# Optimization experiments

Hardware: AMD Instinct MI355X
Metric: run time of the kernel (lower is better)

## Reference

```python
import jax, jax.numpy as jnp
import numpy as np

B, N, K, H = 8, 1024, 16, 4
EMB = 1024

def lrelu(x):
    return jnp.where(x >= 0, x, 0.2 * x)

def bn(x, g, b):
    # eval-mode BatchNorm with running_mean=0, running_var=1
    inv = 1.0 / np.sqrt(1.0 + 1e-5)
    shape = (1, -1) + (1,) * (x.ndim - 2)
    return x * (g * inv).reshape(shape) + b.reshape(shape)

def conv1x1(x, w):
    # 1x1 conv == channel matmul; x: (B,C,...), w: (O,C)
    return jnp.einsum('bc...,oc->bo...', x, w)

def knn_idx(x, k):
    # x: (B,C,N); negative squared pairwise distance, top-k largest = nearest
    inner = -2.0 * jnp.einsum('bcn,bcm->bnm', x, x)
    xx = jnp.sum(x * x, axis=1)                      # (B,N)
    pd = -xx[:, :, None] - inner - xx[:, None, :]
    return jax.lax.top_k(pd, k)[1]                   # (B,N,k)

def graph_feature(x, idx):
    b = x.shape[0]
    xt = jnp.transpose(x, (0, 2, 1))                 # (B,N,C)
    nbr = xt[jnp.arange(b)[:, None, None], idx]      # (B,N,K,C) gather
    ctr = jnp.broadcast_to(xt[:, :, None, :], nbr.shape)
    f = jnp.concatenate([nbr - ctr, ctr], axis=-1)   # (B,N,K,2C)
    return jnp.transpose(f, (0, 3, 1, 2))            # (B,2C,N,K)

def mak(x, y, w0, g0, b0, wm, gm, bm, w1, go, bo, ws, gs, bs, out_ch, in_ch):
    # Multi-head adaptive kernel: generate per-point (out,in,H) weights from y, apply to x
    Bc, _, Nc, Kc = x.shape
    y = lrelu(bn(conv1x1(y, w0), g0, b0))
    y = lrelu(bn(conv1x1(y, wm), gm, bm))
    y = conv1x1(y, w1)                               # (B, out*in*H, N, K)
    w = jnp.transpose(y, (0, 2, 3, 1)).reshape(Bc, Nc, Kc, out_ch, in_ch, H)
    xt = jnp.transpose(x, (0, 2, 3, 1))              # (B,N,K,in)
    # per-head matmul then sum over heads == single einsum over i and h
    out = jnp.einsum('bnkoih,bnki->bonk', w, xt)
    out = bn(out, go, bo)
    idt = bn(conv1x1(x, ws), gs, bs)                 # shortcut (in != out)
    return lrelu(out + idt)


def setup_inputs() -> dict:
    ks = jax.random.split(jax.random.key(0), 48)
    it = iter(range(48))
    def nrm(shape, fan):
        return jax.random.normal(ks[next(it)], shape, jnp.float32) / np.sqrt(fan)
    def gam(c):
        return jax.random.uniform(ks[next(it)], (c,), jnp.float32, 0.5, 1.5)
    def bet(c):
        return 0.1 * jax.random.normal(ks[next(it)], (c,), jnp.float32)
    d = {}
    d['x'] = jax.random.normal(ks[next(it)], (B, 3, N), jnp.float32)
    def mak_params(p, feat_c):
        d[p + '_w0'] = nrm((64, feat_c), feat_c); d[p + '_g0'] = gam(64); d[p + '_b0'] = bet(64)
        d[p + '_wm'] = nrm((64, 64), 64); d[p + '_gm'] = gam(64); d[p + '_bm'] = bet(64)
        d[p + '_w1'] = nrm((64 * 6 * H, 64), 64)
        d[p + '_go'] = gam(64); d[p + '_bo'] = bet(64)
        d[p + '_ws'] = nrm((64, 6), 6); d[p + '_gs'] = gam(64); d[p + '_bs'] = bet(64)
    mak_params('m1', 6)
    mak_params('m2', 128)
    d['w3'] = nrm((128, 128), 128); d['g3'] = gam(128); d['b3'] = bet(128)
    d['w4'] = nrm((256, 256), 256); d['g4'] = gam(256); d['b4'] = bet(256)
    d['w5'] = nrm((EMB, 512), 512); d['g5'] = gam(EMB); d['b5'] = bet(EMB)
    d['wl1'] = nrm((512, 2 * EMB), 2 * EMB); d['bn4_g'] = gam(512); d['bn4_b'] = bet(512)
    d['wl2'] = nrm((256, 512), 512); d['bl2'] = bet(256); d['bn5_g'] = gam(256); d['bn5_b'] = bet(256)
    d['wl3'] = nrm((49, 256), 256); d['bl3'] = bet(49)
    return d


def reference(x, m1_w0, m1_g0, m1_b0, m1_wm, m1_gm, m1_bm, m1_w1, m1_go, m1_bo, m1_ws, m1_gs, m1_bs, m2_w0, m2_g0, m2_b0, m2_wm, m2_gm, m2_bm, m2_w1, m2_go, m2_bo, m2_ws, m2_gs, m2_bs, w3, g3, b3, w4, g4, b4, w5, g5, b5, wl1, bn4_g, bn4_b, wl2, bl2, bn5_g, bn5_b, wl3, bl3):
    idx = knn_idx(x, K)                              # common_idx from points
    geo = graph_feature(x, idx)                      # (B,6,N,K); feat_x == geo_x at stage 1
    h = mak(geo, geo, m1_w0, m1_g0, m1_b0, m1_wm, m1_gm, m1_bm, m1_w1, m1_go, m1_bo, m1_ws, m1_gs, m1_bs, 64, 6)
    x1 = h.max(axis=-1)                              # (B,64,N)
    feat2 = graph_feature(x1, idx)                   # (B,128,N,K)
    h = mak(geo, feat2, m2_w0, m2_g0, m2_b0, m2_wm, m2_gm, m2_bm, m2_w1, m2_go, m2_bo, m2_ws, m2_gs, m2_bs, 64, 6)
    x2 = h.max(axis=-1)                              # (B,64,N)
    x3 = lrelu(bn(conv1x1(graph_feature(x2, idx), w3), g3, b3)).max(axis=-1)   # (B,128,N)
    x4 = lrelu(bn(conv1x1(graph_feature(x3, idx), w4), g4, b4)).max(axis=-1)   # (B,256,N)
    xc = jnp.concatenate([x1, x2, x3, x4], axis=1)   # (B,512,N)
    x5 = lrelu(bn(conv1x1(xc, w5), g5, b5))          # (B,EMB,N)
    xp = jnp.concatenate([x5.max(axis=-1), x5.mean(axis=-1)], axis=1)  # (B,2*EMB)
    xf = lrelu(bn(xp @ wl1.T, bn4_g, bn4_b))
    xf = lrelu(bn(xf @ wl2.T + bl2, bn5_g, bn5_b))
    return xf @ wl3.T + bl3                           # (B,49)
```

## Files before the change

### kernel.cpp

```cpp
#include <hip/hip_runtime.h>
#include <math.h>

#define BB 8
#define NN 1024
#define KK 16
#define NKP (NN*KK)
#define BN_INV 0.99999500003749981f

typedef unsigned short u16;
typedef __attribute__((ext_vector_type(8))) short short8;
typedef __attribute__((ext_vector_type(4))) float f32x4;

#define MFMA16(a,b,c) __builtin_amdgcn_mfma_f32_16x16x32_bf16(a,b,c,0,0,0)

__device__ __forceinline__ float lrelu(float v) { return v >= 0.f ? v : 0.2f * v; }

__device__ __forceinline__ u16 f2bf(float f) {
  union { float f; unsigned u; } v; v.f = f;
  unsigned r = v.u + 0x7fff + ((v.u >> 16) & 1);
  return (u16)(r >> 16);
}
__device__ __forceinline__ float bf2f(u16 s) {
  union { unsigned u; float f; } v; v.u = ((unsigned)s) << 16;
  return v.f;
}

constexpr size_t OFF_IDX   = 0;
constexpr size_t OFF_X1P   = 524288;
constexpr size_t OFF_X2P   = 1572864;
constexpr size_t OFF_X3P   = 2621440;
constexpr size_t OFF_MUV   = 2621440;
constexpr size_t OFF_X4P   = 4718592;
constexpr size_t OFF_GEO   = 4718592;
constexpr size_t OFF_PMAX  = 8912896;
constexpr size_t OFF_PSUM  = 9437184;
constexpr size_t OFF_XP    = 9961472;
constexpr size_t OFF_XF1   = 10027008;
constexpr size_t OFF_XF2   = 10043392;
constexpr size_t OFF_M1WM  = 10055680;
constexpr size_t OFF_M1W1S = 10063872;
constexpr size_t OFF_M2W0S = 10117120;
constexpr size_t OFF_M2WM  = 10133504;
constexpr size_t OFF_M2W1S = 10141696;
constexpr size_t OFF_W3S   = 10194944;
constexpr size_t OFF_W4S   = 10227712;
constexpr size_t OFF_W5    = 10358784;
constexpr size_t OFF_WL1T  = 11407360;
constexpr size_t OFF_WL2T  = 15601664;
constexpr size_t OFF_WL3T  = 16125952;
constexpr size_t OFF_UV3   = 16177152;
constexpr size_t OFF_EY0   = 16177152;
constexpr size_t OFF_UV4   = 20371456;

struct SSeg { const float* w; const float* g; u16* dst; int O; int C; int cpl2; int ch; int stk; int start; };
struct SArgs { SSeg seg[6]; int total; };

__global__ __launch_bounds__(256) void prep_scale_bf16(SArgs a) {
  const int tid = blockIdx.x * 256 + threadIdx.x;
  if (tid >= a.total) return;
  int s = 0;
  #pragma unroll
  for (int i = 1; i < 6; ++i) if (tid >= a.seg[i].start) s = i;
  const SSeg sg = a.seg[s];
  const int e = tid - sg.start;
  const int o2 = e >> sg.cpl2;
  const int c = e & ((1 << sg.cpl2) - 1);
  float v = 0.f;
  if (sg.stk) {
    const int half = sg.O >> 1;
    const int o = o2 & (half - 1);
    const int CIN = 2 * sg.C;
    const float wd = sg.w[o * CIN + c];
    v = (o2 < half) ? wd : (sg.w[o * CIN + sg.C + c] - wd);
    v *= sg.g[o] * BN_INV;
  } else if (c < sg.C) {
    v = sg.w[o2 * sg.C + c];
    if (sg.ch && c >= sg.ch) v -= sg.w[o2 * sg.C + c - sg.ch];
    v *= sg.g[o2] * BN_INV;
  }
  sg.dst[(size_t)(c >> 5) * (sg.O * 32) + o2 * 32 + (c & 31)] = f2bf(v);
}

__global__ __launch_bounds__(256) void prep_w1s_bf16(
    const float* __restrict__ w1a, const float* __restrict__ wsa,
    const float* __restrict__ goa, const float* __restrict__ gsa,
    const float* __restrict__ w1b, const float* __restrict__ wsb,
    const float* __restrict__ gob, const float* __restrict__ gsb,
    u16* __restrict__ dsta, u16* __restrict__ dstb) {
  const int tid = blockIdx.x * 256 + threadIdx.x;
  if (tid >= 64 * 416) return;
  const float* w1 = blockIdx.y ? w1b : w1a;
  const float* wsm = blockIdx.y ? wsb : wsa;
  const float* go = blockIdx.y ? gob : goa;
  const float* gs = blockIdx.y ? gsb : gsa;
  u16* dst = blockIdx.y ? dstb : dsta;
  const int o = tid / 416, ci = tid - o * 416;
  float v = 0.f;
  if (ci < 384) {
    const int ii = ci >> 6, ch = ci & 63;
    const int base = (o * 24 + ii * 4) * 64 + ch;
    v = go[o] * BN_INV * (w1[base] + w1[base + 64] + w1[base + 128] + w1[base + 192]);
  } else if (ci < 390) {
    v = gs[o] * BN_INV * wsm[o * 6 + (ci - 384)];
  }
  dst[(size_t)(ci >> 5) * 2048 + o * 32 + (ci & 31)] = f2bf(v);
}

struct TSeg { const float* w; const float* g; float* dst; int O; int C; int start; };
struct TArgs3 { TSeg seg[3]; int total; };

__global__ __launch_bounds__(256) void prep_transpose_f32(TArgs3 a) {
  const int tid = blockIdx.x * 256 + threadIdx.x;
  if (tid >= a.total) return;
  int s = 0;
  #pragma unroll
  for (int i = 1; i < 3; ++i) if (tid >= a.seg[i].start) s = i;
  const TSeg sg = a.seg[s];
  const int e = tid - sg.start;
  const int c = e / sg.O;
  const int o = e - c * sg.O;
  float v = sg.w[o * sg.C + c];
  if (sg.g) v *= sg.g[o] * BN_INV;
  sg.dst[e] = v;
}

__global__ __launch_bounds__(256) void knn_kernel(const float* __restrict__ x, int* __restrict__ idxout) {
  const int wid  = (blockIdx.x * blockDim.x + threadIdx.x) >> 6;
  const int lane = threadIdx.x & 63;
  const int b = wid >> 10;
  const int n = wid & (NN - 1);
  const float* xb = x + b * 3 * NN;
  const float x0n = xb[n], x1n = xb[NN + n], x2n = xb[2 * NN + n];
  const float xxn = x0n * x0n + x1n * x1n + x2n * x2n;
  float pd[16];
  #pragma unroll
  for (int j = 0; j < 16; ++j) {
    const int m = j * 64 + lane;
    const float x0 = xb[m], x1 = xb[NN + m], x2 = xb[2 * NN + m];
    const float dot = x0n * x0 + x1n * x1 + x2n * x2;
    const float xxm = x0 * x0 + x1 * x1 + x2 * x2;
    pd[j] = 2.f * dot - xxn - xxm;
  }
  for (int r = 0; r < 16; ++r) {
    float bv = pd[0]; int bj = 0;
    #pragma unroll
    for (int j = 1; j < 16; ++j) if (pd[j] > bv) { bv = pd[j]; bj = j; }
    int bm = bj * 64 + lane;
    #pragma unroll
    for (int off = 32; off > 0; off >>= 1) {
      const float ov = __shfl_down(bv, off);
      const int   om = __shfl_down(bm, off);
      if (ov > bv || (ov == bv && om < bm)) { bv = ov; bm = om; }
    }
    bm = __shfl(bm, 0);
    if (lane == 0) idxout[wid * KK + r] = bm;
    const int  cj   = bm >> 6;
    const bool mine = (bm & 63) == lane;
    #pragma unroll
    for (int j = 0; j < 16; ++j) if (mine && j == cj) pd[j] = -INFINITY;
  }
}

__device__ __forceinline__ short8 bfrag64(const u16* T, int pl, int quad, int c0) {
  const int pos = ((c0 >> 3) + quad) ^ (pl & 7);
  return *(const short8*)(T + pl * 64 + pos * 8);
}
__device__ __forceinline__ void writeD64(u16* T, int pl, int quad, const f32x4 a,
                                         const float* __restrict__ bias, int obase) {
  union { ushort4 v; u16 s[4]; } pk;
  #pragma unroll
  for (int r = 0; r < 4; ++r) pk.s[r] = f2bf(lrelu(a[r] + bias[obase + quad * 4 + r]));
  const int g = (obase + quad * 4) >> 3;
  const int pos = g ^ (pl & 7);
  *(ushort4*)(T + pl * 64 + pos * 8 + (quad & 1) * 4) = pk.v;
}

__global__ __launch_bounds__(256) void mak1_uv(
    const float* __restrict__ x, const float* __restrict__ w0,
    const float* __restrict__ g0, const float* __restrict__ b0,
    u16* __restrict__ MUV) {
  const int tid = blockIdx.x * 256 + threadIdx.x;
  if (tid >= BB * NN * 64) return;
  const int o = tid & 63;
  const int p = tid >> 6;
  const int b = p >> 10, n = p & (NN - 1);
  const float* xb = x + b * 3 * NN;
  const float gg = g0[o] * BN_INV;
  float u = 0.f, v = 0.f;
  #pragma unroll
  for (int i = 0; i < 3; ++i) {
    const float wd = w0[o * 6 + i];
    const float wc = w0[o * 6 + 3 + i];
    const float c = xb[i * NN + n];
    u += wd * c;
    v += (wc - wd) * c;
  }
  MUV[(size_t)p * 128 + o]      = f2bf(gg * u);
  MUV[(size_t)p * 128 + 64 + o] = f2bf(gg * v + b0[o]);
}

__global__ __launch_bounds__(256) void mak_edge_build(
    const float* __restrict__ x, const int* __restrict__ idxb,
    const u16* __restrict__ MUV, u16* __restrict__ EY0,
    u16* __restrict__ GEO, int writeGeo) {
  const int tid = blockIdx.x * 256 + threadIdx.x;
  const int cg = tid & 7;
  const int e = tid >> 3;
  const int b = e >> 14;
  const int nk = e & 16383;
  const int n = nk >> 4;
  const int nbr = idxb[e] & (NN - 1);
  union { uint4 q; u16 s[8]; } uu, vv, rr;
  uu.q = *(const uint4*)(MUV + (size_t)(b * NN + nbr) * 128 + cg * 8);
  vv.q = *(const uint4*)(MUV + (size_t)(b * NN + n) * 128 + 64 + cg * 8);
  #pragma unroll
  for (int j = 0; j < 8; ++j) rr.s[j] = f2bf(lrelu(bf2f(uu.s[j]) + bf2f(vv.s[j])));
  *(uint4*)(EY0 + (size_t)e * 64 + cg * 8) = rr.q;
  if (writeGeo && cg == 0) {
    const float* xb = x + b * 3 * NN;
    union { uint4 q; u16 s[8]; } g;
    #pragma unroll
    for (int i = 0; i < 3; ++i) {
      const float fc = xb[i * NN + n];
      g.s[i]     = f2bf(xb[i * NN + nbr] - fc);
      g.s[3 + i] = f2bf(fc);
    }
    g.s[6] = 0; g.s[7] = 0;
    *(uint4*)(GEO + (size_t)e * 8) = g.q;
  }
}

__global__ __launch_bounds__(256, 2) void mak23_mfma(
    const u16* __restrict__ EY0, const u16* __restrict__ GEO,
    const u16* __restrict__ wmb, const float* __restrict__ bmv,
    const u16* __restrict__ w1s, const float* __restrict__ bov, const float* __restrict__ bsv,
    u16* __restrict__ Xoutp) {
  __shared__ __align__(16) u16 YMs[4][64 * 64];

  const int t = threadIdx.x;
  const int b = blockIdx.z;
  const int w = t >> 6, l = t & 63;
  const int quad = l >> 4, l15 = l & 15;
  const int cq8 = quad * 8;
  const int p0 = blockIdx.x * 16 + w * 4;
  u16* myYM = YMs[w];

  float ge[4][6];
  short8 bgv[4];
  size_t eL[4];
  #pragma unroll
  for (int pg = 0; pg < 4; ++pg) {
    eL[pg] = ((size_t)(b * NN + p0 + pg)) * 16 + l15;
    union { short8 v; u16 s[8]; } gq;
    gq.v = *(const short8*)(GEO + eL[pg] * 8);
    #pragma unroll
    for (int ii = 0; ii < 6; ++ii) ge[pg][ii] = bf2f(gq.s[ii]);
    bgv[pg] = (quad == 0) ? gq.v : (short8)(short)0;
  }

  #pragma unroll
  for (int pg = 0; pg < 4; ++pg) {
    f32x4 a2[4];
    #pragma unroll
    for (int i = 0; i < 4; ++i) a2[i] = (f32x4)0.f;
    #pragma unroll
    for (int kc = 0; kc < 2; ++kc) {
      const short8 bf = *(const short8*)(EY0 + eL[pg] * 64 + kc * 32 + cq8);
      #pragma unroll
      for (int at = 0; at < 4; ++at) {
        const short8 af = *(const short8*)(wmb + (size_t)(kc * 64 + at * 16 + l15) * 32 + cq8);
        a2[at] = MFMA16(af, bf, a2[at]);
      }
    }
    #pragma unroll
    for (int at = 0; at < 4; ++at) writeD64(myYM, pg * 16 + l15, quad, a2[at], bmv, at * 16);
  }

  short8 bf3[4][2];
  #pragma unroll
  for (int pg = 0; pg < 4; ++pg)
    #pragma unroll
    for (int kc = 0; kc < 2; ++kc)
      bf3[pg][kc] = bfrag64(myYM, pg * 16 + l15, quad, kc * 32);

  f32x4 acc[4][4];
  #pragma unroll
  for (int pg = 0; pg < 4; ++pg)
    #pragma unroll
    for (int at = 0; at < 4; ++at) acc[pg][at] = (f32x4)0.f;

  #pragma unroll
  for (int ii = 0; ii < 6; ++ii) {
    f32x4 tac[4][4];
    #pragma unroll
    for (int pg = 0; pg < 4; ++pg)
      #pragma unroll
      for (int at = 0; at < 4; ++at) tac[pg][at] = (f32x4)0.f;
    #pragma unroll
    for (int kc = 0; kc < 2; ++kc) {
      #pragma unroll
      for (int at = 0; at < 4; ++at) {
        const short8 af = *(const short8*)(w1s + (size_t)((ii * 2 + kc) * 64 + at * 16 + l15) * 32 + cq8);
        #pragma unroll
        for (int pg = 0; pg < 4; ++pg) tac[pg][at] = MFMA16(af, bf3[pg][kc], tac[pg][at]);
      }
    }
    #pragma unroll
    for (int pg = 0; pg < 4; ++pg) {
      const float g = ge[pg][ii];
      #pragma unroll
      for (int at = 0; at < 4; ++at) acc[pg][at] += g * tac[pg][at];
    }
  }
  #pragma unroll
  for (int at = 0; at < 4; ++at) {
    const short8 af = *(const short8*)(w1s + (size_t)(12 * 64 + at * 16 + l15) * 32 + cq8);
    #pragma unroll
    for (int pg = 0; pg < 4; ++pg) acc[pg][at] = MFMA16(af, bgv[pg], acc[pg][at]);
  }

  #pragma unroll
  for (int pg = 0; pg < 4; ++pg) {
    u16* orow = Xoutp + (size_t)(b * NN + p0 + pg) * 64;
    #pragma unroll
    for (int at = 0; at < 4; ++at) {
      union { ushort4 v; u16 s[4]; } pk;
      #pragma unroll
      for (int r = 0; r < 4; ++r) {
        const int o = at * 16 + quad * 4 + r;
        float v = lrelu(acc[pg][at][r] + bov[o] + bsv[o]);
        v = fmaxf(v, __shfl_xor(v, 1));
        v = fmaxf(v, __shfl_xor(v, 2));
        v = fmaxf(v, __shfl_xor(v, 4));
        v = fmaxf(v, __shfl_xor(v, 8));
        pk.s[r] = f2bf(v);
      }
      if (l15 == 0) *(ushort4*)(orow + at * 16 + quad * 4) = pk.v;
    }
  }
}

template<int CH, int COUT2>
__global__ __launch_bounds__(256) void dense_uv(
    const u16* __restrict__ srcp, const u16* __restrict__ w2,
    const float* __restrict__ bias, u16* __restrict__ UV) {
  constexpr int COUT = COUT2 / 2;
  constexpr int NCH = CH / 32;
  const int t = threadIdx.x;
  const int b = blockIdx.z;
  const int w = t >> 6, l = t & 63;
  const int quad = l >> 4, l15 = l & 15;
  const int cq8 = quad * 8;
  int n0, ow0;
  if constexpr (COUT2 >= 256) { n0 = blockIdx.x * 64; ow0 = blockIdx.y * 256 + w * 64; }
  else { n0 = blockIdx.x * 128 + (w >> 1) * 64; ow0 = (w & 1) * 64; }

  f32x4 acc[4][4];
  #pragma unroll
  for (int i = 0; i < 4; ++i)
    #pragma unroll
    for (int j = 0; j < 4; ++j) acc[i][j] = (f32x4)0.f;

  #pragma unroll
  for (int k = 0; k < NCH; ++k) {
    short8 bfr[4];
    #pragma unroll
    for (int pg = 0; pg < 4; ++pg) {
      const int n = n0 + pg * 16 + l15;
      bfr[pg] = *(const short8*)(srcp + (size_t)(b * NN + n) * CH + k * 32 + cq8);
    }
    #pragma unroll
    for (int at = 0; at < 4; ++at) {
      const short8 af = *(const short8*)(w2 + ((size_t)(k * COUT2 + ow0 + at * 16 + l15)) * 32 + cq8);
      #pragma unroll
      for (int pg = 0; pg < 4; ++pg) acc[at][pg] = MFMA16(af, bfr[pg], acc[at][pg]);
    }
  }

  #pragma unroll
  for (int at = 0; at < 4; ++at) {
    const int o0 = ow0 + at * 16 + quad * 4;
    const bool isv = (o0 >= COUT);
    float bb[4];
    #pragma unroll
    for (int r = 0; r < 4; ++r) bb[r] = isv ? bias[o0 + r - COUT] : 0.f;
    #pragma unroll
    for (int pg = 0; pg < 4; ++pg) {
      const int n = n0 + pg * 16 + l15;
      union { ushort4 v; u16 s[4]; } pk;
      #pragma unroll
      for (int r = 0; r < 4; ++r) pk.s[r] = f2bf(acc[at][pg][r] + bb[r]);
      *(ushort4*)(UV + (size_t)(b * NN + n) * COUT2 + o0) = pk.v;
    }
  }
}

__device__ __forceinline__ float4 ubf4(ushort4 q) {
  float4 f;
  f.x = bf2f(q.x); f.y = bf2f(q.y); f.z = bf2f(q.z); f.w = bf2f(q.w);
  return f;
}

template<int COUT>
__global__ __launch_bounds__(256) void gather_max(
    const u16* __restrict__ UV, const int* __restrict__ idxb,
    u16* __restrict__ Xoutp) {
  constexpr int CG = COUT / 4;
  const int tid = blockIdx.x * 256 + threadIdx.x;
  const int cg = tid & (CG - 1);
  const int P = tid / CG;
  const int b = P >> 10;
  const int n = P & (NN - 1);

  const float4 vv = ubf4(*(const ushort4*)(UV + (size_t)P * (2 * COUT) + COUT + 4 * cg));
  const int4* ip = (const int4*)(idxb + (size_t)b * NKP + n * 16);
  float4 m = {-INFINITY, -INFINITY, -INFINITY, -INFINITY};
  #pragma unroll
  for (int kq = 0; kq < 4; ++kq) {
    const int4 iv = ip[kq];
    const int mr[4] = { iv.x & (NN - 1), iv.y & (NN - 1), iv.z & (NN - 1), iv.w & (NN - 1) };
    ushort4 uq[4];
    #pragma unroll
    for (int j = 0; j < 4; ++j)
      uq[j] = *(const ushort4*)(UV + (size_t)(b * NN + mr[j]) * (2 * COUT) + 4 * cg);
    #pragma unroll
    for (int j = 0; j < 4; ++j) {
      const float4 uu = ubf4(uq[j]);
      float4 s;
      s.x = uu.x + vv.x; s.y = uu.y + vv.y; s.z = uu.z + vv.z; s.w = uu.w + vv.w;
      m.x = fmaxf(m.x, fmaxf(s.x, 0.2f * s.x));
      m.y = fmaxf(m.y, fmaxf(s.y, 0.2f * s.y));
      m.z = fmaxf(m.z, fmaxf(s.z, 0.2f * s.z));
      m.w = fmaxf(m.w, fmaxf(s.w, 0.2f * s.w));
    }
  }
  union { ushort4 v; u16 s[4]; } pk;
  pk.s[0] = f2bf(m.x); pk.s[1] = f2bf(m.y); pk.s[2] = f2bf(m.z); pk.s[3] = f2bf(m.w);
  *(ushort4*)(Xoutp + (size_t)P * COUT + 4 * cg) = pk.v;
}

__global__ __launch_bounds__(256) void conv5_mfma(
    const u16* __restrict__ X1P, const u16* __restrict__ X2P,
    const u16* __restrict__ X3P, const u16* __restrict__ X4P,
    const u16* __restrict__ w5b, const float* __restrict__ b5,
    float* __restrict__ PMAX, float* __restrict__ PSUM) {
  const int t = threadIdx.x;
  const int b = blockIdx.z;
  const int n0 = blockIdx.x * 64;
  const int w = t >> 6, l = t & 63;
  const int quad = l >> 4, l15 = l & 15;
  const int cq8 = quad * 8;
  const int ow0 = blockIdx.y * 256 + w * 64;

  f32x4 acc[4][4];
  #pragma unroll
  for (int i = 0; i < 4; ++i)
    #pragma unroll
    for (int j = 0; j < 4; ++j) acc[i][j] = (f32x4)0.f;

  #pragma unroll 4
  for (int k = 0; k < 16; ++k) {
    const int c = k * 32 + cq8;
    short8 bfr[4];
    #pragma unroll
    for (int pg = 0; pg < 4; ++pg) {
      const int n = n0 + pg * 16 + l15;
      const u16* src; int cc;
      if (c < 64)       { src = X1P + (size_t)(b * NN + n) * 64;  cc = c; }
      else if (c < 128) { src = X2P + (size_t)(b * NN + n) * 64;  cc = c - 64; }
      else if (c < 256) { src = X3P + (size_t)(b * NN + n) * 128; cc = c - 128; }
      else              { src = X4P + (size_t)(b * NN + n) * 256; cc = c - 256; }
      bfr[pg] = *(const short8*)(src + cc);
    }
    #pragma unroll
    for (int at = 0; at < 4; ++at) {
      const short8 af = *(const short8*)(w5b + ((size_t)(k * 1024 + ow0 + at * 16 + l15)) * 32 + cq8);
      #pragma unroll
      for (int pg = 0; pg < 4; ++pg) acc[at][pg] = MFMA16(af, bfr[pg], acc[at][pg]);
    }
  }

  #pragma unroll
  for (int at = 0; at < 4; ++at) {
    f32x4 pmx, psm;
    #pragma unroll
    for (int r = 0; r < 4; ++r) {
      const float bb = b5[ow0 + at * 16 + quad * 4 + r];
      float m = -INFINITY, s = 0.f;
      #pragma unroll
      for (int pg = 0; pg < 4; ++pg) {
        const float v = lrelu(acc[at][pg][r] + bb);
        m = fmaxf(m, v); s += v;
      }
      #pragma unroll
      for (int msk = 1; msk < 16; msk <<= 1) {
        m = fmaxf(m, __shfl_xor(m, msk));
        s += __shfl_xor(s, msk);
      }
      pmx[r] = m; psm[r] = s;
    }
    if (l15 == 0) {
      float* dm = PMAX + (size_t)(b * 16 + blockIdx.x) * 1024 + ow0 + at * 16 + quad * 4;
      float* ds = PSUM + (size_t)(b * 16 + blockIdx.x) * 1024 + ow0 + at * 16 + quad * 4;
      *(f32x4*)dm = pmx;
      *(f32x4*)ds = psm;
    }
  }
}

__global__ __launch_bounds__(256) void reduce5(const float* __restrict__ PMAX, const float* __restrict__ PSUM,
                                               float* __restrict__ XPg) {
  const int tid = blockIdx.x * 256 + threadIdx.x;
  const int b = tid >> 10, o = tid & 1023;
  float m = -INFINITY, s = 0.f;
  for (int pt = 0; pt < 16; ++pt) {
    m = fmaxf(m, PMAX[(size_t)(b * 16 + pt) * 1024 + o]);
    s += PSUM[(size_t)(b * 16 + pt) * 1024 + o];
  }
  XPg[b * 2048 + o] = m;
  XPg[b * 2048 + 1024 + o] = s * (1.f / 1024.f);
}

__global__ __launch_bounds__(256) void fc1_kernel(const float* __restrict__ XPg, const float* __restrict__ wl1t,
                                                  const float* __restrict__ bn4_b, float* __restrict__ XF1) {
  __shared__ float red[64 * 5];
  const int t = threadIdx.x;
  const int b = blockIdx.y;
  const int o = blockIdx.x * 64 + (t & 63);
  const int cq = t >> 6;
  const float* xp = XPg + b * 2048;
  float acc = 0.f;
  for (int c = cq * 512; c < cq * 512 + 512; ++c) acc = fmaf(wl1t[c * 512 + o], xp[c], acc);
  red[(t & 63) * 5 + cq] = acc;
  __syncthreads();
  if (t < 64) {
    const int oo = blockIdx.x * 64 + t;
    const float v = red[t * 5] + red[t * 5 + 1] + red[t * 5 + 2] + red[t * 5 + 3] + bn4_b[oo];
    XF1[b * 512 + oo] = lrelu(v);
  }
}

__global__ __launch_bounds__(256) void fc2_kernel(const float* __restrict__ XF1, const float* __restrict__ wl2t,
                                                  const float* __restrict__ bl2, const float* __restrict__ bn5_g,
                                                  const float* __restrict__ bn5_b, float* __restrict__ XF2) {
  __shared__ float red[64 * 5];
  const int t = threadIdx.x;
  const int b = blockIdx.y;
  const int o = blockIdx.x * 64 + (t & 63);
  const int cq = t >> 6;
  const float* xf = XF1 + b * 512;
  float acc = 0.f;
  for (int c = cq * 128; c < cq * 128 + 128; ++c) acc = fmaf(wl2t[c * 256 + o], xf[c], acc);
  red[(t & 63) * 5 + cq] = acc;
  __syncthreads();
  if (t < 64) {
    const int oo = blockIdx.x * 64 + t;
    const float bias = bl2[oo] * (bn5_g[oo] * BN_INV) + bn5_b[oo];
    const float v = red[t * 5] + red[t * 5 + 1] + red[t * 5 + 2] + red[t * 5 + 3] + bias;
    XF2[b * 256 + oo] = lrelu(v);
  }
}

__global__ __launch_bounds__(256) void fc3_kernel(const float* __restrict__ XF2, const float* __restrict__ wl3t,
                                                  const float* __restrict__ bl3, float* __restrict__ out) {
  __shared__ float red[64 * 5];
  const int t = threadIdx.x;
  const int b = blockIdx.y;
  const int ol = t & 63;
  const int cq = t >> 6;
  const float* xf = XF2 + b * 256;
  float acc = 0.f;
  if (ol < 49) for (int c = cq * 64; c < cq * 64 + 64; ++c) acc = fmaf(wl3t[c * 49 + ol], xf[c], acc);
  red[ol * 5 + cq] = acc;
  __syncthreads();
  if (t < 49) out[b * 49 + t] = red[t * 5] + red[t * 5 + 1] + red[t * 5 + 2] + red[t * 5 + 3] + bl3[t];
}

extern "C" void kernel_launch(void* const* d_in, const int* in_sizes, int n_in,
                              void* d_out, int out_size, void* d_ws, size_t ws_size,
                              hipStream_t stream) {
  (void)in_sizes; (void)n_in; (void)out_size; (void)ws_size;
  const float* x     = (const float*)d_in[0];
  const float* m1_w0 = (const float*)d_in[1];
  const float* m1_g0 = (const float*)d_in[2];
  const float* m1_b0 = (const float*)d_in[3];
  const float* m1_wm = (const float*)d_in[4];
  const float* m1_gm = (const float*)d_in[5];
  const float* m1_bm = (const float*)d_in[6];
  const float* m1_w1 = (const float*)d_in[7];
  const float* m1_go = (const float*)d_in[8];
  const float* m1_bo = (const float*)d_in[9];
  const float* m1_ws = (const float*)d_in[10];
  const float* m1_gs = (const float*)d_in[11];
  const float* m1_bs = (const float*)d_in[12];
  const float* m2_w0 = (const float*)d_in[13];
  const float* m2_g0 = (const float*)d_in[14];
  const float* m2_b0 = (const float*)d_in[15];
  const float* m2_wm = (const float*)d_in[16];
  const float* m2_gm = (const float*)d_in[17];
  const float* m2_bm = (const float*)d_in[18];
  const float* m2_w1 = (const float*)d_in[19];
  const float* m2_go = (const float*)d_in[20];
  const float* m2_bo = (const float*)d_in[21];
  const float* m2_ws = (const float*)d_in[22];
  const float* m2_gs = (const float*)d_in[23];
  const float* m2_bs = (const float*)d_in[24];
  const float* w3    = (const float*)d_in[25];
  const float* g3    = (const float*)d_in[26];
  const float* b3    = (const float*)d_in[27];
  const float* w4    = (const float*)d_in[28];
  const float* g4    = (const float*)d_in[29];
  const float* b4    = (const float*)d_in[30];
  const float* w5    = (const float*)d_in[31];
  const float* g5    = (const float*)d_in[32];
  const float* b5    = (const float*)d_in[33];
  const float* wl1   = (const float*)d_in[34];
  const float* bn4_g = (const float*)d_in[35];
  const float* bn4_b = (const float*)d_in[36];
  const float* wl2   = (const float*)d_in[37];
  const float* bl2   = (const float*)d_in[38];
  const float* bn5_g = (const float*)d_in[39];
  const float* bn5_b = (const float*)d_in[40];
  const float* wl3   = (const float*)d_in[41];
  const float* bl3   = (const float*)d_in[42];

  char* wsb = (char*)d_ws;
  int*  IDX  = (int*)(wsb + OFF_IDX);
  u16*  X1P  = (u16*)(wsb + OFF_X1P);
  u16*  X2P  = (u16*)(wsb + OFF_X2P);
  u16*  X3P  = (u16*)(wsb + OFF_X3P);
  u16*  X4P  = (u16*)(wsb + OFF_X4P);
  u16*  MUV  = (u16*)(wsb + OFF_MUV);
  u16*  GEO  = (u16*)(wsb + OFF_GEO);
  u16*  EY0  = (u16*)(wsb + OFF_EY0);
  float* PMAX = (float*)(wsb + OFF_PMAX);
  float* PSUM = (float*)(wsb + OFF_PSUM);
  float* XPg  = (float*)(wsb + OFF_XP);
  float* XF1  = (float*)(wsb + OFF_XF1);
  float* XF2  = (float*)(wsb + OFF_XF2);
  u16*  M1WM = (u16*)(wsb + OFF_M1WM);
  u16*  M1W1S = (u16*)(wsb + OFF_M1W1S);
  u16*  M2W0S = (u16*)(wsb + OFF_M2W0S);
  u16*  M2WM = (u16*)(wsb + OFF_M2WM);
  u16*  M2W1S = (u16*)(wsb + OFF_M2W1S);
  u16*  W3S  = (u16*)(wsb + OFF_W3S);
  u16*  W4S  = (u16*)(wsb + OFF_W4S);
  u16*  W5B  = (u16*)(wsb + OFF_W5);
  float* WL1T = (float*)(wsb + OFF_WL1T);
  float* WL2T = (float*)(wsb + OFF_WL2T);
  float* WL3T = (float*)(wsb + OFF_WL3T);
  u16*  UV3  = (u16*)(wsb + OFF_UV3);
  u16*  UV4  = (u16*)(wsb + OFF_UV4);

  SArgs sa; int st = 0;
  auto sset = [&](int i, const float* w, const float* g, u16* dst, int O, int C, int cpl2, int ch, int stk) {
    sa.seg[i].w = w; sa.seg[i].g = g; sa.seg[i].dst = dst; sa.seg[i].O = O; sa.seg[i].C = C;
    sa.seg[i].cpl2 = cpl2; sa.seg[i].ch = ch; sa.seg[i].stk = stk; sa.seg[i].start = st;
    st += O << cpl2;
  };
  sset(0, m1_wm, m1_gm, M1WM, 64, 64, 6, 0, 0);
  sset(1, m2_w0, m2_g0, M2W0S, 128, 64, 6, 0, 1);
  sset(2, m2_wm, m2_gm, M2WM, 64, 64, 6, 0, 0);
  sset(3, w3, g3, W3S, 256, 64, 6, 0, 1);
  sset(4, w4, g4, W4S, 512, 128, 7, 0, 1);
  sset(5, w5, g5, W5B, 1024, 512, 9, 0, 0);
  sa.total = st;

  TArgs3 ta; int tt = 0;
  auto tset = [&](int i, const float* w, const float* g, float* dst, int O, int C) {
    ta.seg[i].w = w; ta.seg[i].g = g; ta.seg[i].dst = dst; ta.seg[i].O = O; ta.seg[i].C = C;
    ta.seg[i].start = tt; tt += O * C;
  };
  tset(0, wl1, bn4_g, WL1T, 512, 2048);
  tset(1, wl2, bn5_g, WL2T, 256, 512);
  tset(2, wl3, nullptr, WL3T, 49, 256);
  ta.total = tt;

  hipLaunchKernelGGL(prep_scale_bf16, dim3((sa.total + 255) / 256), dim3(256), 0, stream, sa);
  hipLaunchKernelGGL(prep_w1s_bf16, dim3(104, 2), dim3(256), 0, stream,
                     m1_w1, m1_ws, m1_go, m1_gs, m2_w1, m2_ws, m2_go, m2_gs, M1W1S, M2W1S);
  hipLaunchKernelGGL(prep_transpose_f32, dim3((ta.total + 255) / 256), dim3(256), 0, stream, ta);

  hipLaunchKernelGGL(knn_kernel, dim3(2048), dim3(256), 0, stream, x, IDX);

  hipLaunchKernelGGL(mak1_uv, dim3((BB * NN * 64 + 255) / 256), dim3(256), 0, stream,
                     x, m1_w0, m1_g0, m1_b0, MUV);
  hipLaunchKernelGGL(mak_edge_build, dim3(4096), dim3(256), 0, stream, x, IDX, MUV, EY0, GEO, 1);
  hipLaunchKernelGGL(mak23_mfma, dim3(64, 1, BB), dim3(256), 0, stream,
                     EY0, GEO, M1WM, m1_bm, M1W1S, m1_bo, m1_bs, X1P);

  hipLaunchKernelGGL((dense_uv<64, 128>), dim3(8, 1, BB), dim3(256), 0, stream, X1P, M2W0S, m2_b0, MUV);
  hipLaunchKernelGGL(mak_edge_build, dim3(4096), dim3(256), 0, stream, x, IDX, MUV, EY0, GEO, 0);
  hipLaunchKernelGGL(mak23_mfma, dim3(64, 1, BB), dim3(256), 0, stream,
                     EY0, GEO, M2WM, m2_bm, M2W1S, m2_bo, m2_bs, X2P);

  hipLaunchKernelGGL((dense_uv<64, 256>), dim3(16, 1, BB), dim3(256), 0, stream, X2P, W3S, b3, UV3);
  hipLaunchKernelGGL((gather_max<128>), dim3(1024), dim3(256), 0, stream, UV3, IDX, X3P);
  hipLaunchKernelGGL((dense_uv<128, 512>), dim3(16, 2, BB), dim3(256), 0, stream, X3P, W4S, b4, UV4);
  hipLaunchKernelGGL((gather_max<256>), dim3(2048), dim3(256), 0, stream, UV4, IDX, X4P);

  hipLaunchKernelGGL(conv5_mfma, dim3(16, 4, BB), dim3(256), 0, stream,
                     X1P, X2P, X3P, X4P, W5B, b5, PMAX, PSUM);
  hipLaunchKernelGGL(reduce5, dim3(32), dim3(256), 0, stream, PMAX, PSUM, XPg);

  hipLaunchKernelGGL(fc1_kernel, dim3(8, BB), dim3(256), 0, stream, XPg, WL1T, bn4_b, XF1);
  hipLaunchKernelGGL(fc2_kernel, dim3(4, BB), dim3(256), 0, stream, XF1, WL2T, bl2, bn5_g, bn5_b, XF2);
  hipLaunchKernelGGL(fc3_kernel, dim3(1, BB), dim3(256), 0, stream, XF2, WL3T, bl3, (float*)d_out);
}
```

Baseline: 384.3 us.

## Fuse edge-feature build into MAK MFMA kernel, dropping EY0/GEO buffers

Removes the separate mak_edge_build kernel and computes the gathered edge activations (lrelu of u[nbr]+v[ctr]) and geometric features directly inside mak23_mfma from MUV, x and the kNN indices. This avoids writing and re-reading the large intermediate EY0 and GEO buffers and drops two kernel launches. The first-layer MFMA loop is reordered so each weight fragment is reused across four point groups. The cost is more registers in a kernel already launched with bounds of 2 blocks per SM, and gather latency now sits inside the compute kernel.

```diff
diff --git a/kernel.cpp b/kernel.cpp
--- a/kernel.cpp
+++ b/kernel.cpp
@@ -31,7 +31,6 @@
 constexpr size_t OFF_X3P   = 2621440;
 constexpr size_t OFF_MUV   = 2621440;
 constexpr size_t OFF_X4P   = 4718592;
-constexpr size_t OFF_GEO   = 4718592;
 constexpr size_t OFF_PMAX  = 8912896;
 constexpr size_t OFF_PSUM  = 9437184;
 constexpr size_t OFF_XP    = 9961472;
@@ -49,7 +48,6 @@
 constexpr size_t OFF_WL2T  = 15601664;
 constexpr size_t OFF_WL3T  = 16125952;
 constexpr size_t OFF_UV3   = 16177152;
-constexpr size_t OFF_EY0   = 16177152;
 constexpr size_t OFF_UV4   = 20371456;
 
 struct SSeg { const float* w; const float* g; u16* dst; int O; int C; int cpl2; int ch; int stk; int start; };
@@ -199,39 +197,8 @@
   MUV[(size_t)p * 128 + 64 + o] = f2bf(gg * v + b0[o]);
 }
 
-__global__ __launch_bounds__(256) void mak_edge_build(
-    const float* __restrict__ x, const int* __restrict__ idxb,
-    const u16* __restrict__ MUV, u16* __restrict__ EY0,
-    u16* __restrict__ GEO, int writeGeo) {
-  const int tid = blockIdx.x * 256 + threadIdx.x;
-  const int cg = tid & 7;
-  const int e = tid >> 3;
-  const int b = e >> 14;
-  const int nk = e & 16383;
-  const int n = nk >> 4;
-  const int nbr = idxb[e] & (NN - 1);
-  union { uint4 q; u16 s[8]; } uu, vv, rr;
-  uu.q = *(const uint4*)(MUV + (size_t)(b * NN + nbr) * 128 + cg * 8);
-  vv.q = *(const uint4*)(MUV + (size_t)(b * NN + n) * 128 + 64 + cg * 8);
-  #pragma unroll
-  for (int j = 0; j < 8; ++j) rr.s[j] = f2bf(lrelu(bf2f(uu.s[j]) + bf2f(vv.s[j])));
-  *(uint4*)(EY0 + (size_t)e * 64 + cg * 8) = rr.q;
-  if (writeGeo && cg == 0) {
-    const float* xb = x + b * 3 * NN;
-    union { uint4 q; u16 s[8]; } g;
-    #pragma unroll
-    for (int i = 0; i < 3; ++i) {
-      const float fc = xb[i * NN + n];
-      g.s[i]     = f2bf(xb[i * NN + nbr] - fc);
-      g.s[3 + i] = f2bf(fc);
-    }
-    g.s[6] = 0; g.s[7] = 0;
-    *(uint4*)(GEO + (size_t)e * 8) = g.q;
-  }
-}
-
 __global__ __launch_bounds__(256, 2) void mak23_mfma(
-    const u16* __restrict__ EY0, const u16* __restrict__ GEO,
+    const float* __restrict__ x, const int* __restrict__ idxb, const u16* __restrict__ MUV,
     const u16* __restrict__ wmb, const float* __restrict__ bmv,
     const u16* __restrict__ w1s, const float* __restrict__ bov, const float* __restrict__ bsv,
     u16* __restrict__ Xoutp) {
@@ -244,36 +211,60 @@
   const int cq8 = quad * 8;
   const int p0 = blockIdx.x * 16 + w * 4;
   u16* myYM = YMs[w];
+  const float* xb = x + b * 3 * NN;
+
+  int nbr[4];
+  #pragma unroll
+  for (int pg = 0; pg < 4; ++pg)
+    nbr[pg] = idxb[(size_t)(b * NN + p0 + pg) * 16 + l15] & (NN - 1);
 
   float ge[4][6];
   short8 bgv[4];
-  size_t eL[4];
   #pragma unroll
   for (int pg = 0; pg < 4; ++pg) {
-    eL[pg] = ((size_t)(b * NN + p0 + pg)) * 16 + l15;
+    const int ctr = p0 + pg;
     union { short8 v; u16 s[8]; } gq;
-    gq.v = *(const short8*)(GEO + eL[pg] * 8);
-    #pragma unroll
-    for (int ii = 0; ii < 6; ++ii) ge[pg][ii] = bf2f(gq.s[ii]);
+    gq.v = (short8)(short)0;
+    #pragma unroll
+    for (int i = 0; i < 3; ++i) {
+      const float fc = xb[i * NN + ctr];
+      ge[pg][i]     = xb[i * NN + nbr[pg]] - fc;
+      ge[pg][3 + i] = fc;
+      gq.s[i]     = f2bf(ge[pg][i]);
+      gq.s[3 + i] = f2bf(ge[pg][3 + i]);
+    }
     bgv[pg] = (quad == 0) ? gq.v : (short8)(short)0;
   }
 
+  short8 bf[4][2];
   #pragma unroll
   for (int pg = 0; pg < 4; ++pg) {
+    const u16* urow = MUV + (size_t)(b * NN + nbr[pg]) * 128;
+    const u16* vrow = MUV + (size_t)(b * NN + p0 + pg) * 128 + 64;
+    #pragma unroll
+    for (int kc = 0; kc < 2; ++kc) {
+      union { short8 v; u16 s[8]; } uu, vv, rr;
+      uu.v = *(const short8*)(urow + kc * 32 + cq8);
+      vv.v = *(const short8*)(vrow + kc * 32 + cq8);
+      #pragma unroll
+      for (int j = 0; j < 8; ++j) rr.s[j] = f2bf(lrelu(bf2f(uu.s[j]) + bf2f(vv.s[j])));
+      bf[pg][kc] = rr.v;
+    }
+  }
+
+  #pragma unroll
+  for (int at = 0; at < 4; ++at) {
     f32x4 a2[4];
     #pragma unroll
-    for (int i = 0; i < 4; ++i) a2[i] = (f32x4)0.f;
+    for (int pg = 0; pg < 4; ++pg) a2[pg] = (f32x4)0.f;
     #pragma unroll
     for (int kc = 0; kc < 2; ++kc) {
-      const short8 bf = *(const short8*)(EY0 + eL[pg] * 64 + kc * 32 + cq8);
-      #pragma unroll
-      for (int at = 0; at < 4; ++at) {
-        const short8 af = *(const short8*)(wmb + (size_t)(kc * 64 + at * 16 + l15) * 32 + cq8);
-        a2[at] = MFMA16(af, bf, a2[at]);
-      }
-    }
-    #pragma unroll
-    for (int at = 0; at < 4; ++at) writeD64(myYM, pg * 16 + l15, quad, a2[at], bmv, at * 16);
+      const short8 af = *(const short8*)(wmb + (size_t)(kc * 64 + at * 16 + l15) * 32 + cq8);
+      #pragma unroll
+      for (int pg = 0; pg < 4; ++pg) a2[pg] = MFMA16(af, bf[pg][kc], a2[pg]);
+    }
+    #pragma unroll
+    for (int pg = 0; pg < 4; ++pg) writeD64(myYM, pg * 16 + l15, quad, a2[pg], bmv, at * 16);
   }
 
   short8 bf3[4][2];
@@ -631,8 +622,6 @@
   u16*  X3P  = (u16*)(wsb + OFF_X3P);
   u16*  X4P  = (u16*)(wsb + OFF_X4P);
   u16*  MUV  = (u16*)(wsb + OFF_MUV);
-  u16*  GEO  = (u16*)(wsb + OFF_GEO);
-  u16*  EY0  = (u16*)(wsb + OFF_EY0);
   float* PMAX = (float*)(wsb + OFF_PMAX);
   float* PSUM = (float*)(wsb + OFF_PSUM);
   float* XPg  = (float*)(wsb + OFF_XP);
@@ -685,14 +674,12 @@
 
   hipLaunchKernelGGL(mak1_uv, dim3((BB * NN * 64 + 255) / 256), dim3(256), 0, stream,
                      x, m1_w0, m1_g0, m1_b0, MUV);
-  hipLaunchKernelGGL(mak_edge_build, dim3(4096), dim3(256), 0, stream, x, IDX, MUV, EY0, GEO, 1);
   hipLaunchKernelGGL(mak23_mfma, dim3(64, 1, BB), dim3(256), 0, stream,
-                     EY0, GEO, M1WM, m1_bm, M1W1S, m1_bo, m1_bs, X1P);
+                     x, IDX, MUV, M1WM, m1_bm, M1W1S, m1_bo, m1_bs, X1P);
 
   hipLaunchKernelGGL((dense_uv<64, 128>), dim3(8, 1, BB), dim3(256), 0, stream, X1P, M2W0S, m2_b0, MUV);
-  hipLaunchKernelGGL(mak_edge_build, dim3(4096), dim3(256), 0, stream, x, IDX, MUV, EY0, GEO, 0);
   hipLaunchKernelGGL(mak23_mfma, dim3(64, 1, BB), dim3(256), 0, stream,
-                     EY0, GEO, M2WM, m2_bm, M2W1S, m2_bo, m2_bs, X2P);
+                     x, IDX, MUV, M2WM, m2_bm, M2W1S, m2_bo, m2_bs, X2P);
 
   hipLaunchKernelGGL((dense_uv<64, 256>), dim3(16, 1, BB), dim3(256), 0, stream, X2P, W3S, b3, UV3);
   hipLaunchKernelGGL((gather_max<128>), dim3(1024), dim3(256), 0, stream, UV3, IDX, X3P);
```

New measurement: 362.8 us. -5.6%, faster.
